# Kernel optimization log

Hardware: AMD Instinct MI355X
Metric: run time of the kernel (lower is better)

## Reference

```python
import jax, jax.numpy as jnp
import numpy as np

B, S, D, H = 8, 1024, 1024, 16
HD = D // H
EPS = 1e-06


def setup_inputs() -> dict:
    key = jax.random.key(0)
    ks = jax.random.split(key, 10)
    sc = 0.02
    inp = {
        "y": jax.random.normal(ks[0], (B, S, D), dtype=jnp.float32),
        "y_mask": jax.random.randint(ks[1], (B, 1, 1, S), 0, 2) == 1,
        "Wq": jax.random.normal(ks[2], (D, D), dtype=jnp.float32) * sc,
        "bq": jnp.zeros((D,), jnp.float32),
        "Wk": jax.random.normal(ks[3], (D, D), dtype=jnp.float32) * sc,
        "bk": jnp.zeros((D,), jnp.float32),
        "Wv": jax.random.normal(ks[4], (D, D), dtype=jnp.float32) * sc,
        "bv": jnp.zeros((D,), jnp.float32),
        "Wm": jax.random.normal(ks[5], (D, D), dtype=jnp.float32) * sc,
        "bm": jnp.zeros((D,), jnp.float32),
        "a2": jnp.ones((D,), jnp.float32),
        "b2": jnp.zeros((D,), jnp.float32),
    }
    return inp


def _heads(x):
    # [B,S,D] -> [B,H,S,HD]
    return x.reshape(B, S, H, HD).transpose(0, 2, 1, 3)


def reference(y, y_mask, Wq, bq, Wk, bk, Wv, bv, Wm, bm, a2, b2):
    # torch Linear: x @ W^T + b
    q = _heads(y @ Wq.T + bq)
    k = _heads(y @ Wk.T + bk)
    v = _heads(y @ Wv.T + bv)
    scores = jnp.einsum("bhqd,bhkd->bhqk", q, k) / jnp.sqrt(jnp.float32(HD))
    scores = jnp.where(y_mask, jnp.float32(-1e9), scores)
    att = jax.nn.softmax(scores, axis=-1)  # dropout = identity in eval
    atted = jnp.einsum("bhqk,bhkd->bhqd", att, v)
    atted = atted.transpose(0, 2, 1, 3).reshape(B, S, D)
    atted = atted @ Wm.T + bm
    x = y + atted  # residual (dropout1 = identity in eval)
    mean = x.mean(-1, keepdims=True)
    # torch std: unbiased (ddof=1); eps added to std, not variance
    std = jnp.sqrt(((x - mean) ** 2).sum(-1, keepdims=True) / jnp.float32(D - 1))
    return a2 * (x - mean) / (std + EPS) + b2
```

## Files before the change

### kernel.cpp

```cpp
#include <hip/hip_runtime.h>

#define DEVFN __device__ __forceinline__

typedef unsigned short u16;
typedef __attribute__((ext_vector_type(8))) unsigned short u16x8;
typedef __attribute__((ext_vector_type(4))) unsigned short u16x4;
typedef __attribute__((ext_vector_type(8))) __bf16 bf16x8;
typedef __attribute__((ext_vector_type(4))) float f32x4;

DEVFN u16 f2bf(float f) {
    unsigned u = __builtin_bit_cast(unsigned, f);
    u += 0x7FFFu + ((u >> 16) & 1u);
    return (u16)(u >> 16);
}

DEVFN u16 f2bf_hw(float f) {
    return __builtin_bit_cast(u16, (__bf16)f);
}

DEVFN float bf2f(u16 h) {
    unsigned u = (unsigned)h << 16;
    return __builtin_bit_cast(float, u);
}

DEVFN bf16x8 ldfrag(const u16* p) {
    return __builtin_bit_cast(bf16x8, *(const u16x8*)p);
}

DEVFN f32x4 mfma16(bf16x8 a, bf16x8 b, f32x4 c) {
    return __builtin_amdgcn_mfma_f32_16x16x32_bf16(a, b, c, 0, 0, 0);
}

DEVFN void async16(const u16* g, u16* l) {
    __builtin_amdgcn_global_load_lds(
        (const __attribute__((address_space(1))) void*)g,
        (__attribute__((address_space(3))) void*)l, 16, 0, 0);
}

__global__ __launch_bounds__(256) void conv_all(const float* __restrict__ y,
                                                const float* __restrict__ w0,
                                                const float* __restrict__ w1,
                                                const float* __restrict__ w2,
                                                const float* __restrict__ w3,
                                                u16* __restrict__ yb,
                                                u16* __restrict__ wb) {
    const int b = blockIdx.x;
    const float* src;
    u16* dst;
    int idx;
    if (b < 8192) {
        src = y; dst = yb;
        idx = b * 1024 + threadIdx.x * 4;
    } else {
        const int g = (b - 8192) >> 10;
        src = g == 0 ? w0 : (g == 1 ? w1 : (g == 2 ? w2 : w3));
        dst = wb + (size_t)g * 1024 * 1024;
        idx = ((b - 8192) & 1023) * 1024 + threadIdx.x * 4;
    }
    const float4 v = *(const float4*)&src[idx];
    u16x4 o;
    o.x = f2bf(v.x); o.y = f2bf(v.y); o.z = f2bf(v.z); o.w = f2bf(v.w);
    *(u16x4*)&dst[idx] = o;
}

__global__ __launch_bounds__(256) void gemm_bt(const u16* __restrict__ A,
                                               const u16* __restrict__ Bt,
                                               const float* __restrict__ b0,
                                               const float* __restrict__ b1,
                                               const float* __restrict__ b2,
                                               u16* __restrict__ C0,
                                               u16* __restrict__ C1,
                                               u16* __restrict__ C2,
                                               int K) {
    __shared__ u16 lA[2][128 * 32];
    __shared__ u16 lB[2][128 * 32];
    const int tid = threadIdx.x;
    const int wave = tid >> 6, lane = tid & 63;
    const int quad = lane >> 4, l16 = lane & 15;
    const int n0 = blockIdx.x * 128, m0 = blockIdx.y * 128;
    const int wm = (wave >> 1) * 64, wn = (wave & 1) * 64;
    const int srow = tid >> 2, scol = (tid & 3) * 8;
    const u16* Ag = A + (size_t)(m0 + srow) * K + scol;
    const u16* Bg = Bt + (size_t)(n0 + srow) * K + scol;
    f32x4 acc[4][4] = {};
    for (int k0 = 0; k0 < K; k0 += 64) {
        __syncthreads();
        #pragma unroll
        for (int h = 0; h < 2; ++h)
            #pragma unroll
            for (int c = 0; c < 2; ++c) {
                async16(Ag + k0 + h * 32 + (size_t)(c * 64) * K,
                        &lA[h][c * 2048 + wave * 512]);
                async16(Bg + k0 + h * 32 + (size_t)(c * 64) * K,
                        &lB[h][c * 2048 + wave * 512]);
            }
        __syncthreads();
        #pragma unroll
        for (int kh = 0; kh < 2; ++kh) {
            bf16x8 af[4], bfr[4];
            #pragma unroll
            for (int i = 0; i < 4; ++i)
                af[i] = ldfrag(&lA[kh][(wm + i * 16 + l16) * 32 + quad * 8]);
            #pragma unroll
            for (int i = 0; i < 4; ++i)
                bfr[i] = ldfrag(&lB[kh][(wn + i * 16 + l16) * 32 + quad * 8]);
            #pragma unroll
            for (int mi = 0; mi < 4; ++mi)
                #pragma unroll
                for (int ni = 0; ni < 4; ++ni)
                    acc[mi][ni] = mfma16(af[mi], bfr[ni], acc[mi][ni]);
        }
    }
    #pragma unroll
    for (int mi = 0; mi < 4; ++mi) {
        #pragma unroll
        for (int ni = 0; ni < 4; ++ni) {
            const int col = n0 + wn + ni * 16 + l16;
            const int cs = col >> 10;
            const int c = col & 1023;
            const float* bp = cs == 0 ? b0 : (cs == 1 ? b1 : b2);
            u16* cp = cs == 0 ? C0 : (cs == 1 ? C1 : C2);
            const float bb = bp[c];
            #pragma unroll
            for (int r = 0; r < 4; ++r) {
                const int row = m0 + wm + mi * 16 + quad * 4 + r;
                cp[(size_t)row * 1024 + c] = f2bf(acc[mi][ni][r] + bb);
            }
        }
    }
}

__global__ __launch_bounds__(256) void transpose_v(const u16* __restrict__ v,
                                                   u16* __restrict__ vt) {
    const int bh = blockIdx.y, bb = bh >> 4, h = bh & 15;
    const int s0 = blockIdx.x * 64;
    __shared__ u16 t[64 * 72];
    const int r = threadIdx.x >> 3, c8 = (threadIdx.x & 7) * 8;
    #pragma unroll
    for (int rr = 0; rr < 64; rr += 32)
        *(u16x8*)&t[(r + rr) * 72 + c8] =
            *(const u16x8*)&v[(size_t)(bb * 1024 + s0 + r + rr) * 1024 + h * 64 + c8];
    __syncthreads();
    #pragma unroll
    for (int rr = 0; rr < 64; rr += 32) {
        u16x8 o;
        #pragma unroll
        for (int j = 0; j < 8; ++j) o[j] = t[(c8 + j) * 72 + (r + rr)];
        *(u16x8*)&vt[(size_t)(bh * 64 + r + rr) * 1024 + s0 + c8] = o;
    }
}

__global__ __launch_bounds__(256) void attn(const u16* __restrict__ qb,
                                            const u16* __restrict__ kb,
                                            const u16* __restrict__ vtb,
                                            const int* __restrict__ mask,
                                            u16* __restrict__ attb) {
    const int lin = blockIdx.x;
    const int xcd = lin & 7, slot = lin >> 3;
    const int bh = xcd * 16 + (slot >> 3);
    const int q0 = (slot & 7) * 128;
    const int bb = bh >> 4, h = bh & 15;
    const int tid = threadIdx.x, wave = tid >> 6, lane = tid & 63;
    const int quad = lane >> 4, l16 = lane & 15;
    __shared__ u16 lK[64 * 72];
    __shared__ u16 lV[64 * 72];
    __shared__ u16 lP[128 * 72];
    __shared__ float lM[1024];

    const int* mrow = mask + bb * 1024;
    for (int i = tid; i < 1024; i += 256) lM[i] = mrow[i] ? -1e9f : 0.0f;

    bf16x8 aq[2][2];
    #pragma unroll
    for (int rg = 0; rg < 2; ++rg) {
        const int qrow = q0 + wave * 32 + rg * 16 + l16;
        const u16* qp = qb + (size_t)(bb * 1024 + qrow) * 1024 + h * 64 + quad * 8;
        aq[rg][0] = ldfrag(qp);
        aq[rg][1] = ldfrag(qp + 32);
    }

    f32x4 o[2][4] = {};
    float ps_acc[2][4] = {};

    const int srow = tid >> 3, scol = (tid & 7) * 8;
    const u16* kbase = kb + (size_t)(bb * 1024) * 1024 + h * 64 + scol;
    const u16* vbase = vtb + (size_t)(bh * 64 + srow) * 1024 + scol;

    u16x8 nk0 = *(const u16x8*)(kbase + (size_t)srow * 1024);
    u16x8 nk1 = *(const u16x8*)(kbase + (size_t)(srow + 32) * 1024);
    u16x8 nv0 = *(const u16x8*)(vbase);
    u16x8 nv1 = *(const u16x8*)(vbase + (size_t)32 * 1024);

    const float C = 0.18033688011112043f;

    for (int kt = 0; kt < 1024; kt += 64) {
        __syncthreads();
        *(u16x8*)&lK[srow * 72 + scol] = nk0;
        *(u16x8*)&lK[(srow + 32) * 72 + scol] = nk1;
        *(u16x8*)&lV[srow * 72 + scol] = nv0;
        *(u16x8*)&lV[(srow + 32) * 72 + scol] = nv1;
        __syncthreads();
        const int ktn = kt + 64;
        if (ktn < 1024) {
            nk0 = *(const u16x8*)(kbase + (size_t)(ktn + srow) * 1024);
            nk1 = *(const u16x8*)(kbase + (size_t)(ktn + srow + 32) * 1024);
            nv0 = *(const u16x8*)(vbase + ktn);
            nv1 = *(const u16x8*)(vbase + (size_t)32 * 1024 + ktn);
        }

        bf16x8 kf[4][2];
        #pragma unroll
        for (int n = 0; n < 4; ++n) {
            kf[n][0] = ldfrag(&lK[(n * 16 + l16) * 72 + quad * 8]);
            kf[n][1] = ldfrag(&lK[(n * 16 + l16) * 72 + 32 + quad * 8]);
        }
        f32x4 s[2][4];
        #pragma unroll
        for (int rg = 0; rg < 2; ++rg)
            #pragma unroll
            for (int n = 0; n < 4; ++n) {
                f32x4 t = {};
                t = mfma16(aq[rg][0], kf[n][0], t);
                t = mfma16(aq[rg][1], kf[n][1], t);
                s[rg][n] = t;
            }
        float bias[4];
        #pragma unroll
        for (int n = 0; n < 4; ++n) bias[n] = lM[kt + n * 16 + l16];
        #pragma unroll
        for (int rg = 0; rg < 2; ++rg)
            #pragma unroll
            for (int n = 0; n < 4; ++n)
                #pragma unroll
                for (int r = 0; r < 4; ++r) {
                    const float p =
                        __builtin_amdgcn_exp2f(__builtin_fmaf(s[rg][n][r], C, bias[n]));
                    ps_acc[rg][r] += p;
                    lP[(wave * 32 + rg * 16 + quad * 4 + r) * 72 + n * 16 + l16] =
                        f2bf_hw(p);
                }
        __asm__ __volatile__("s_waitcnt lgkmcnt(0)" ::: "memory");
        bf16x8 ap[2][2];
        #pragma unroll
        for (int rg = 0; rg < 2; ++rg) {
            ap[rg][0] = ldfrag(&lP[(wave * 32 + rg * 16 + l16) * 72 + quad * 8]);
            ap[rg][1] = ldfrag(&lP[(wave * 32 + rg * 16 + l16) * 72 + 32 + quad * 8]);
        }
        bf16x8 vf[4][2];
        #pragma unroll
        for (int ni = 0; ni < 4; ++ni) {
            vf[ni][0] = ldfrag(&lV[(ni * 16 + l16) * 72 + quad * 8]);
            vf[ni][1] = ldfrag(&lV[(ni * 16 + l16) * 72 + 32 + quad * 8]);
        }
        #pragma unroll
        for (int rg = 0; rg < 2; ++rg)
            #pragma unroll
            for (int ni = 0; ni < 4; ++ni) {
                o[rg][ni] = mfma16(ap[rg][0], vf[ni][0], o[rg][ni]);
                o[rg][ni] = mfma16(ap[rg][1], vf[ni][1], o[rg][ni]);
            }
    }
    #pragma unroll
    for (int off = 1; off < 16; off <<= 1)
        #pragma unroll
        for (int rg = 0; rg < 2; ++rg)
            #pragma unroll
            for (int r = 0; r < 4; ++r)
                ps_acc[rg][r] += __shfl_xor(ps_acc[rg][r], off);
    float rl[2][4];
    #pragma unroll
    for (int rg = 0; rg < 2; ++rg)
        #pragma unroll
        for (int r = 0; r < 4; ++r) rl[rg][r] = 1.f / ps_acc[rg][r];
    #pragma unroll
    for (int rg = 0; rg < 2; ++rg)
        #pragma unroll
        for (int ni = 0; ni < 4; ++ni)
            #pragma unroll
            for (int r = 0; r < 4; ++r) {
                const int row = q0 + wave * 32 + rg * 16 + quad * 4 + r;
                attb[(size_t)(bb * 1024 + row) * 1024 + h * 64 + ni * 16 + l16] =
                    f2bf_hw(o[rg][ni][r] * rl[rg][r]);
            }
}

__global__ __launch_bounds__(256) void ln_res(const float* __restrict__ y,
                                              const u16* __restrict__ xpb,
                                              const float* __restrict__ a2,
                                              const float* __restrict__ b2,
                                              float* __restrict__ out) {
    const int row = blockIdx.x, tid = threadIdx.x;
    const size_t base = (size_t)row * 1024;
    const int j = tid * 4;
    const float4 yv = *(const float4*)&y[base + j];
    const u16x4 xv = *(const u16x4*)&xpb[base + j];
    float x[4] = {yv.x + bf2f(xv.x), yv.y + bf2f(xv.y),
                  yv.z + bf2f(xv.z), yv.w + bf2f(xv.w)};
    float s = 0.f, ss = 0.f;
    #pragma unroll
    for (int i = 0; i < 4; ++i) { s += x[i]; ss += x[i] * x[i]; }
    #pragma unroll
    for (int off = 1; off < 64; off <<= 1) {
        s += __shfl_xor(s, off);
        ss += __shfl_xor(ss, off);
    }
    __shared__ float rs[4], rss[4];
    const int wave = tid >> 6, lane = tid & 63;
    if (lane == 0) { rs[wave] = s; rss[wave] = ss; }
    __syncthreads();
    s = rs[0] + rs[1] + rs[2] + rs[3];
    ss = rss[0] + rss[1] + rss[2] + rss[3];
    const float mean = s * (1.f / 1024.f);
    float var = (ss - s * mean) * (1.f / 1023.f);
    var = fmaxf(var, 0.f);
    const float inv = 1.f / (sqrtf(var) + 1e-6f);
    const float4 av = *(const float4*)&a2[j];
    const float4 bv = *(const float4*)&b2[j];
    float4 ov;
    ov.x = av.x * (x[0] - mean) * inv + bv.x;
    ov.y = av.y * (x[1] - mean) * inv + bv.y;
    ov.z = av.z * (x[2] - mean) * inv + bv.z;
    ov.w = av.w * (x[3] - mean) * inv + bv.w;
    *(float4*)&out[base + j] = ov;
}

extern "C" void kernel_launch(void* const* d_in, const int* in_sizes, int n_in,
                              void* d_out, int out_size, void* d_ws, size_t ws_size,
                              hipStream_t stream) {
    (void)in_sizes; (void)n_in; (void)out_size;
    const float* y   = (const float*)d_in[0];
    const int*   msk = (const int*)d_in[1];
    const float* Wq  = (const float*)d_in[2];
    const float* bq  = (const float*)d_in[3];
    const float* Wk  = (const float*)d_in[4];
    const float* bkb = (const float*)d_in[5];
    const float* Wv  = (const float*)d_in[6];
    const float* bv  = (const float*)d_in[7];
    const float* Wm  = (const float*)d_in[8];
    const float* bm  = (const float*)d_in[9];
    const float* a2  = (const float*)d_in[10];
    const float* b2  = (const float*)d_in[11];
    float* out = (float*)d_out;

    char* ws = (char*)d_ws;
    const size_t MB = 1u << 20;
    if (ws_size < 72 * MB) return;
    u16* yb  = (u16*)(ws);
    u16* wqb = (u16*)(ws + 16 * MB);
    u16* wmb = (u16*)(ws + 22 * MB);
    u16* qb  = (u16*)(ws + 24 * MB);
    u16* kb  = (u16*)(ws + 40 * MB);
    u16* vb  = (u16*)(ws + 56 * MB);
    u16* vtb  = yb;
    u16* attb = vb;
    u16* xpb  = qb;

    conv_all<<<12288, 256, 0, stream>>>(y, Wq, Wk, Wv, Wm, yb, wqb);

    gemm_bt<<<dim3(24, 64), 256, 0, stream>>>(
        yb, wqb, bq, bkb, bv, qb, kb, vb, 1024);

    transpose_v<<<dim3(16, 128), 256, 0, stream>>>(vb, vtb);
    attn<<<dim3(1024), 256, 0, stream>>>(qb, kb, vtb, msk, attb);

    gemm_bt<<<dim3(8, 64), 256, 0, stream>>>(
        attb, wmb, bm, bm, bm, xpb, xpb, xpb, 1024);
    ln_res<<<8192, 256, 0, stream>>>(y, xpb, a2, b2, out);
}
```

Before: 293.0 us.

## Compact unmasked key indices and skip masked keys in attention

A new kernel compacts each batch's mask into a list of unmasked key positions plus a count. The V transpose and the attention kernel then gather only those keys and stop the key loop at the rounded-up count, so masked keys are never loaded or multiplied. The padding tail inside the last tile is masked arithmetically instead of through a shared-memory mask table. Separately, the GEMM drops from a 64-wide double-slab K step to a single 32-wide slab per iteration, which halves its LDS use but doubles its barrier count. The index scratch lives in the output buffer before the final layernorm overwrites it. A fully masked row would now produce a zero softmax denominator instead of the reference's uniform weights.

```diff
diff --git a/kernel.cpp b/kernel.cpp
--- a/kernel.cpp
+++ b/kernel.cpp
@@ -63,6 +63,26 @@
     *(u16x4*)&dst[idx] = o;
 }
 
+__global__ __launch_bounds__(64) void compact_mask(const int* __restrict__ mask,
+                                                   int* __restrict__ idx,
+                                                   int* __restrict__ cnt) {
+    const int b = blockIdx.x;
+    const int lane = threadIdx.x;
+    const int* m = mask + b * 1024;
+    int* ib = idx + b * 1024;
+    int base = 0;
+    for (int t = 0; t < 16; ++t) {
+        const int pos = t * 64 + lane;
+        const int valid = (m[pos] == 0) ? 1 : 0;
+        const unsigned long long bal = __ballot(valid);
+        const int pre = __popcll(bal & ((1ull << lane) - 1ull));
+        if (valid) ib[base + pre] = pos;
+        base += (int)__popcll(bal);
+    }
+    if (lane == 0) cnt[b] = base;
+    for (int i = base + lane; i < 1024; i += 64) ib[i] = 0;
+}
+
 __global__ __launch_bounds__(256) void gemm_bt(const u16* __restrict__ A,
                                                const u16* __restrict__ Bt,
                                                const float* __restrict__ b0,
@@ -72,44 +92,42 @@
                                                u16* __restrict__ C1,
                                                u16* __restrict__ C2,
                                                int K) {
-    __shared__ u16 lA[2][128 * 32];
-    __shared__ u16 lB[2][128 * 32];
+    __shared__ u16 lA[128 * 32];
+    __shared__ u16 lB[128 * 32];
     const int tid = threadIdx.x;
     const int wave = tid >> 6, lane = tid & 63;
     const int quad = lane >> 4, l16 = lane & 15;
     const int n0 = blockIdx.x * 128, m0 = blockIdx.y * 128;
     const int wm = (wave >> 1) * 64, wn = (wave & 1) * 64;
     const int srow = tid >> 2, scol = (tid & 3) * 8;
-    const u16* Ag = A + (size_t)(m0 + srow) * K + scol;
-    const u16* Bg = Bt + (size_t)(n0 + srow) * K + scol;
+    const u16* Ag0 = A + (size_t)(m0 + srow) * K + scol;
+    const u16* Ag1 = A + (size_t)(m0 + 64 + srow) * K + scol;
+    const u16* Bg0 = Bt + (size_t)(n0 + srow) * K + scol;
+    const u16* Bg1 = Bt + (size_t)(n0 + 64 + srow) * K + scol;
+    u16* lA0 = &lA[wave * 512];
+    u16* lA1 = &lA[2048 + wave * 512];
+    u16* lB0 = &lB[wave * 512];
+    u16* lB1 = &lB[2048 + wave * 512];
     f32x4 acc[4][4] = {};
-    for (int k0 = 0; k0 < K; k0 += 64) {
+    for (int k0 = 0; k0 < K; k0 += 32) {
         __syncthreads();
-        #pragma unroll
-        for (int h = 0; h < 2; ++h)
-            #pragma unroll
-            for (int c = 0; c < 2; ++c) {
-                async16(Ag + k0 + h * 32 + (size_t)(c * 64) * K,
-                        &lA[h][c * 2048 + wave * 512]);
-                async16(Bg + k0 + h * 32 + (size_t)(c * 64) * K,
-                        &lB[h][c * 2048 + wave * 512]);
-            }
+        async16(Ag0 + k0, lA0);
+        async16(Ag1 + k0, lA1);
+        async16(Bg0 + k0, lB0);
+        async16(Bg1 + k0, lB1);
         __syncthreads();
-        #pragma unroll
-        for (int kh = 0; kh < 2; ++kh) {
-            bf16x8 af[4], bfr[4];
-            #pragma unroll
-            for (int i = 0; i < 4; ++i)
-                af[i] = ldfrag(&lA[kh][(wm + i * 16 + l16) * 32 + quad * 8]);
-            #pragma unroll
-            for (int i = 0; i < 4; ++i)
-                bfr[i] = ldfrag(&lB[kh][(wn + i * 16 + l16) * 32 + quad * 8]);
-            #pragma unroll
-            for (int mi = 0; mi < 4; ++mi)
-                #pragma unroll
-                for (int ni = 0; ni < 4; ++ni)
-                    acc[mi][ni] = mfma16(af[mi], bfr[ni], acc[mi][ni]);
-        }
+        bf16x8 af[4], bfr[4];
+        #pragma unroll
+        for (int i = 0; i < 4; ++i)
+            af[i] = ldfrag(&lA[(wm + i * 16 + l16) * 32 + quad * 8]);
+        #pragma unroll
+        for (int i = 0; i < 4; ++i)
+            bfr[i] = ldfrag(&lB[(wn + i * 16 + l16) * 32 + quad * 8]);
+        #pragma unroll
+        for (int mi = 0; mi < 4; ++mi)
+            #pragma unroll
+            for (int ni = 0; ni < 4; ++ni)
+                acc[mi][ni] = mfma16(af[mi], bfr[ni], acc[mi][ni]);
     }
     #pragma unroll
     for (int mi = 0; mi < 4; ++mi) {
@@ -130,16 +148,22 @@
     }
 }
 
-__global__ __launch_bounds__(256) void transpose_v(const u16* __restrict__ v,
-                                                   u16* __restrict__ vt) {
+__global__ __launch_bounds__(256) void transpose_vc(const u16* __restrict__ v,
+                                                    u16* __restrict__ vt,
+                                                    const int* __restrict__ idx,
+                                                    const int* __restrict__ cnt) {
     const int bh = blockIdx.y, bb = bh >> 4, h = bh & 15;
     const int s0 = blockIdx.x * 64;
+    const int cn = cnt[bb];
+    if (s0 >= ((cn + 63) & ~63)) return;
     __shared__ u16 t[64 * 72];
     const int r = threadIdx.x >> 3, c8 = (threadIdx.x & 7) * 8;
     #pragma unroll
-    for (int rr = 0; rr < 64; rr += 32)
+    for (int rr = 0; rr < 64; rr += 32) {
+        const int src = idx[bb * 1024 + s0 + r + rr];
         *(u16x8*)&t[(r + rr) * 72 + c8] =
-            *(const u16x8*)&v[(size_t)(bb * 1024 + s0 + r + rr) * 1024 + h * 64 + c8];
+            *(const u16x8*)&v[(size_t)(bb * 1024 + src) * 1024 + h * 64 + c8];
+    }
     __syncthreads();
     #pragma unroll
     for (int rr = 0; rr < 64; rr += 32) {
@@ -153,7 +177,8 @@
 __global__ __launch_bounds__(256) void attn(const u16* __restrict__ qb,
                                             const u16* __restrict__ kb,
                                             const u16* __restrict__ vtb,
-                                            const int* __restrict__ mask,
+                                            const int* __restrict__ idxb,
+                                            const int* __restrict__ cntb,
                                             u16* __restrict__ attb) {
     const int lin = blockIdx.x;
     const int xcd = lin & 7, slot = lin >> 3;
@@ -165,10 +190,10 @@
     __shared__ u16 lK[64 * 72];
     __shared__ u16 lV[64 * 72];
     __shared__ u16 lP[128 * 72];
-    __shared__ float lM[1024];
-
-    const int* mrow = mask + bb * 1024;
-    for (int i = tid; i < 1024; i += 256) lM[i] = mrow[i] ? -1e9f : 0.0f;
+
+    const int cn = cntb[bb];
+    const int kEnd = (cn + 63) & ~63;
+    const int* ib = idxb + bb * 1024;
 
     bf16x8 aq[2][2];
     #pragma unroll
@@ -186,14 +211,15 @@
     const u16* kbase = kb + (size_t)(bb * 1024) * 1024 + h * 64 + scol;
     const u16* vbase = vtb + (size_t)(bh * 64 + srow) * 1024 + scol;
 
-    u16x8 nk0 = *(const u16x8*)(kbase + (size_t)srow * 1024);
-    u16x8 nk1 = *(const u16x8*)(kbase + (size_t)(srow + 32) * 1024);
+    int gi0 = ib[srow], gi1 = ib[srow + 32];
+    u16x8 nk0 = *(const u16x8*)(kbase + (size_t)gi0 * 1024);
+    u16x8 nk1 = *(const u16x8*)(kbase + (size_t)gi1 * 1024);
     u16x8 nv0 = *(const u16x8*)(vbase);
     u16x8 nv1 = *(const u16x8*)(vbase + (size_t)32 * 1024);
 
     const float C = 0.18033688011112043f;
 
-    for (int kt = 0; kt < 1024; kt += 64) {
+    for (int kt = 0; kt < kEnd; kt += 64) {
         __syncthreads();
         *(u16x8*)&lK[srow * 72 + scol] = nk0;
         *(u16x8*)&lK[(srow + 32) * 72 + scol] = nk1;
@@ -201,9 +227,10 @@
         *(u16x8*)&lV[(srow + 32) * 72 + scol] = nv1;
         __syncthreads();
         const int ktn = kt + 64;
-        if (ktn < 1024) {
-            nk0 = *(const u16x8*)(kbase + (size_t)(ktn + srow) * 1024);
-            nk1 = *(const u16x8*)(kbase + (size_t)(ktn + srow + 32) * 1024);
+        if (ktn < kEnd) {
+            gi0 = ib[ktn + srow]; gi1 = ib[ktn + srow + 32];
+            nk0 = *(const u16x8*)(kbase + (size_t)gi0 * 1024);
+            nk1 = *(const u16x8*)(kbase + (size_t)gi1 * 1024);
             nv0 = *(const u16x8*)(vbase + ktn);
             nv1 = *(const u16x8*)(vbase + (size_t)32 * 1024 + ktn);
         }
@@ -226,7 +253,8 @@
             }
         float bias[4];
         #pragma unroll
-        for (int n = 0; n < 4; ++n) bias[n] = lM[kt + n * 16 + l16];
+        for (int n = 0; n < 4; ++n)
+            bias[n] = (kt + n * 16 + l16 < cn) ? 0.0f : -1e9f;
         #pragma unroll
         for (int rg = 0; rg < 2; ++rg)
             #pragma unroll
@@ -355,13 +383,17 @@
     u16* attb = vb;
     u16* xpb  = qb;
 
+    int* idxb = (int*)d_out;
+    int* cntb = idxb + 8192;
+
     conv_all<<<12288, 256, 0, stream>>>(y, Wq, Wk, Wv, Wm, yb, wqb);
+    compact_mask<<<8, 64, 0, stream>>>(msk, idxb, cntb);
 
     gemm_bt<<<dim3(24, 64), 256, 0, stream>>>(
         yb, wqb, bq, bkb, bv, qb, kb, vb, 1024);
 
-    transpose_v<<<dim3(16, 128), 256, 0, stream>>>(vb, vtb);
-    attn<<<dim3(1024), 256, 0, stream>>>(qb, kb, vtb, msk, attb);
+    transpose_vc<<<dim3(16, 128), 256, 0, stream>>>(vb, vtb, idxb, cntb);
+    attn<<<dim3(1024), 256, 0, stream>>>(qb, kb, vtb, idxb, cntb, attb);
 
     gemm_bt<<<dim3(8, 64), 256, 0, stream>>>(
         attb, wmb, bm, bm, bm, xpb, xpb, xpb, 1024);
```

Measured after the change: 277.3 us. 5.4% less time.
